# Kernel optimization log

Measured on AMD Instinct MI355X. Metric: run time of the kernel, lower is better.

The kernel has to match this reference:

```python
import jax, jax.numpy as jnp
import numpy as np

B, S, E = 4, 2048, 1024
N, H = 16, 64  # n_head, per-head hidden


def setup_inputs() -> dict:
    key = jax.random.key(0)
    k1, k2, k3, k4, k5 = jax.random.split(key, 5)
    scale_in = 1.0 / np.sqrt(E)
    scale_h = 1.0 / np.sqrt(N * H)
    return {
        "x": jax.random.normal(k1, (B, S, E), dtype=jnp.float32),
        "W_qkv": jax.random.uniform(k2, (E, 3 * N * H), minval=-scale_in, maxval=scale_in, dtype=jnp.float32),
        "b_qkv": jax.random.uniform(k3, (3 * N * H,), minval=-scale_in, maxval=scale_in, dtype=jnp.float32),
        "W_out": jax.random.uniform(k4, (N * H, E), minval=-scale_h, maxval=scale_h, dtype=jnp.float32),
        "b_out": jax.random.uniform(k5, (E,), minval=-scale_h, maxval=scale_h, dtype=jnp.float32),
    }


def reference(x, W_qkv, b_qkv, W_out, b_out):
    b, s, e = x.shape
    qkv = x @ W_qkv + b_qkv                      # [B,S,3NH]
    q, k, v = jnp.split(qkv, 3, axis=-1)
    q = q.reshape(b, s, N, H).transpose(0, 2, 1, 3)  # [B,N,S,H]
    k = k.reshape(b, s, N, H).transpose(0, 2, 1, 3)
    v = v.reshape(b, s, N, H).transpose(0, 2, 1, 3)
    inv_scale = jnp.asarray(1.0 / np.sqrt(H), dtype=x.dtype)
    attn = jnp.einsum('bnqh,bnkh->bnqk', q, k) * inv_scale  # [B,N,S,S]
    causal = jnp.tril(jnp.ones((s, s), dtype=bool))
    attn = jnp.where(causal[None, None], attn, jnp.asarray(-jnp.inf, dtype=attn.dtype))
    attn = jax.nn.softmax(attn, axis=-1)
    out = jnp.einsum('bnqk,bnkh->bnqh', attn, v)  # [B,N,S,H]
    out = out.transpose(0, 2, 1, 3).reshape(b, s, N * H)
    return out @ W_out + b_out
```

## Files before the change

### kernel.cpp

```cpp
#include <hip/hip_runtime.h>
#include <hip/hip_bf16.h>

typedef __attribute__((ext_vector_type(8))) short s16x8;
typedef __attribute__((ext_vector_type(4))) short s16x4;
typedef __attribute__((ext_vector_type(4))) float f32x4;

#define MFMA16(a, b, c) __builtin_amdgcn_mfma_f32_16x16x32_bf16(a, b, c, 0, 0, 0)

__device__ __forceinline__ short f2bf(float f) {
  unsigned int x = __builtin_bit_cast(unsigned int, f);
  x += 0x7fffu + ((x >> 16) & 1u);
  return (short)(x >> 16);
}

__device__ __forceinline__ int cperm(int k) {
  return ((k & 12) << 1) | ((k >> 4) << 2) | (k & 3);
}

#define LDT 40

__global__ void cvt_f32_bf16(const float* __restrict__ in, short* __restrict__ out, int n) {
  int idx = blockIdx.x * blockDim.x + threadIdx.x;
  int stride = gridDim.x * blockDim.x;
  for (int i = idx * 4; i < n; i += stride * 4) {
    float4 v = *(const float4*)(in + i);
    s16x4 o;
    o[0] = f2bf(v.x); o[1] = f2bf(v.y); o[2] = f2bf(v.z); o[3] = f2bf(v.w);
    *(s16x4*)(out + i) = o;
  }
}

__global__ __launch_bounds__(256) void gemm_qkv(
    const short* __restrict__ X, const short* __restrict__ W,
    const float* __restrict__ bias,
    short* __restrict__ Qo, short* __restrict__ Ko, short* __restrict__ Vo) {
  const int N = 3072, Kd = 1024;
  __shared__ short As[128 * LDT];
  __shared__ short Bs[128 * LDT];
  int t = threadIdx.x;
  int nTN = N / 128;
  int m0 = (blockIdx.x / nTN) * 128;
  int n0 = (blockIdx.x % nTN) * 128;
  int lane = t & 63, w = t >> 6;
  int wr = (w >> 1) * 64, wc = (w & 1) * 64;
  int r = lane & 15, g = lane >> 4;

  int ar = t >> 1;
  int ak = (t & 1) << 4;
  int bk = t & 31;
  int bc = (t >> 5) << 4;
  int cbk = cperm(bk);

  f32x4 acc[4][4];
  const f32x4 z4 = {0.f, 0.f, 0.f, 0.f};
#pragma unroll
  for (int i = 0; i < 4; ++i)
#pragma unroll
    for (int j = 0; j < 4; ++j) acc[i][j] = z4;

  for (int kt = 0; kt < Kd; kt += 32) {
    if (kt) __syncthreads();
    const short* xr = X + (size_t)(m0 + ar) * Kd + kt + ak;
    s16x8 va0 = *(const s16x8*)(xr);
    s16x8 va1 = *(const s16x8*)(xr + 8);
    short* Ad = &As[ar * LDT];
    *(s16x4*)(Ad + cperm(ak))      = __builtin_shufflevector(va0, va0, 0, 1, 2, 3);
    *(s16x4*)(Ad + cperm(ak + 4))  = __builtin_shufflevector(va0, va0, 4, 5, 6, 7);
    *(s16x4*)(Ad + cperm(ak + 8))  = __builtin_shufflevector(va1, va1, 0, 1, 2, 3);
    *(s16x4*)(Ad + cperm(ak + 12)) = __builtin_shufflevector(va1, va1, 4, 5, 6, 7);
    const short* wrp = W + (size_t)(kt + bk) * N + n0 + bc;
    s16x8 vb0 = *(const s16x8*)(wrp);
    s16x8 vb1 = *(const s16x8*)(wrp + 8);
#pragma unroll
    for (int i = 0; i < 8; ++i) Bs[(bc + i) * LDT + cbk] = vb0[i];
#pragma unroll
    for (int i = 0; i < 8; ++i) Bs[(bc + 8 + i) * LDT + cbk] = vb1[i];
    __syncthreads();

    s16x8 af[4], bfr[4];
#pragma unroll
    for (int mi = 0; mi < 4; ++mi)
      af[mi] = *(const s16x8*)(&As[(wr + mi * 16 + r) * LDT + g * 8]);
#pragma unroll
    for (int ni = 0; ni < 4; ++ni)
      bfr[ni] = *(const s16x8*)(&Bs[(wc + ni * 16 + r) * LDT + g * 8]);
#pragma unroll
    for (int mi = 0; mi < 4; ++mi)
#pragma unroll
      for (int ni = 0; ni < 4; ++ni)
        acc[mi][ni] = MFMA16(af[mi], bfr[ni], acc[mi][ni]);
  }

#pragma unroll
  for (int ni = 0; ni < 4; ++ni) {
    int col = n0 + wc + ni * 16 + r;
    float bv = bias[col];
    int which = col >> 10;
    int rem = col & 1023;
    int head = rem >> 6, h = rem & 63;
    short* dst = (which == 0) ? Qo : (which == 1) ? Ko : Vo;
    float qsc = (which == 0) ? 0.125f : 1.0f;
#pragma unroll
    for (int mi = 0; mi < 4; ++mi)
#pragma unroll
      for (int e = 0; e < 4; ++e) {
        int row = m0 + wr + mi * 16 + g * 4 + e;
        int b = row >> 11, s = row & 2047;
        dst[((size_t)(b * 16 + head) * 2048 + s) * 64 + h] = f2bf((acc[mi][ni][e] + bv) * qsc);
      }
  }
}

__global__ __launch_bounds__(256) void gemm_out(
    const short* __restrict__ X, const short* __restrict__ W,
    const float* __restrict__ bias, float* __restrict__ Out) {
  const int N = 1024, Kd = 1024;
  __shared__ short As[128 * LDT];
  __shared__ short Bs[128 * LDT];
  int t = threadIdx.x;
  int nTN = N / 128;
  int m0 = (blockIdx.x / nTN) * 128;
  int n0 = (blockIdx.x % nTN) * 128;
  int lane = t & 63, w = t >> 6;
  int wr = (w >> 1) * 64, wc = (w & 1) * 64;
  int r = lane & 15, g = lane >> 4;
  int ar = t >> 1, ak = (t & 1) << 4;
  int bk = t & 31, bc = (t >> 5) << 4;
  int cbk = cperm(bk);

  f32x4 acc[4][4];
  const f32x4 z4 = {0.f, 0.f, 0.f, 0.f};
#pragma unroll
  for (int i = 0; i < 4; ++i)
#pragma unroll
    for (int j = 0; j < 4; ++j) acc[i][j] = z4;

  for (int kt = 0; kt < Kd; kt += 32) {
    if (kt) __syncthreads();
    const short* xr = X + (size_t)(m0 + ar) * Kd + kt + ak;
    s16x8 va0 = *(const s16x8*)(xr);
    s16x8 va1 = *(const s16x8*)(xr + 8);
    short* Ad = &As[ar * LDT];
    *(s16x4*)(Ad + cperm(ak))      = __builtin_shufflevector(va0, va0, 0, 1, 2, 3);
    *(s16x4*)(Ad + cperm(ak + 4))  = __builtin_shufflevector(va0, va0, 4, 5, 6, 7);
    *(s16x4*)(Ad + cperm(ak + 8))  = __builtin_shufflevector(va1, va1, 0, 1, 2, 3);
    *(s16x4*)(Ad + cperm(ak + 12)) = __builtin_shufflevector(va1, va1, 4, 5, 6, 7);
    const short* wrp = W + (size_t)(kt + bk) * N + n0 + bc;
    s16x8 vb0 = *(const s16x8*)(wrp);
    s16x8 vb1 = *(const s16x8*)(wrp + 8);
#pragma unroll
    for (int i = 0; i < 8; ++i) Bs[(bc + i) * LDT + cbk] = vb0[i];
#pragma unroll
    for (int i = 0; i < 8; ++i) Bs[(bc + 8 + i) * LDT + cbk] = vb1[i];
    __syncthreads();

    s16x8 af[4], bfr[4];
#pragma unroll
    for (int mi = 0; mi < 4; ++mi)
      af[mi] = *(const s16x8*)(&As[(wr + mi * 16 + r) * LDT + g * 8]);
#pragma unroll
    for (int ni = 0; ni < 4; ++ni)
      bfr[ni] = *(const s16x8*)(&Bs[(wc + ni * 16 + r) * LDT + g * 8]);
#pragma unroll
    for (int mi = 0; mi < 4; ++mi)
#pragma unroll
      for (int ni = 0; ni < 4; ++ni)
        acc[mi][ni] = MFMA16(af[mi], bfr[ni], acc[mi][ni]);
  }

#pragma unroll
  for (int ni = 0; ni < 4; ++ni) {
    int col = n0 + wc + ni * 16 + r;
    float bv = bias[col];
#pragma unroll
    for (int mi = 0; mi < 4; ++mi)
#pragma unroll
      for (int e = 0; e < 4; ++e) {
        int row = m0 + wr + mi * 16 + g * 4 + e;
        Out[(size_t)row * N + col] = acc[mi][ni][e] + bv;
      }
  }
}

#define LDTV 72
__global__ __launch_bounds__(256) void attn(
    const short* __restrict__ Qb, const short* __restrict__ Kb,
    const short* __restrict__ Vb, short* __restrict__ Ob) {
  const int S = 2048, H = 64;
  int bid = blockIdx.x;
  int bn = bid & 63;
  int pr = bid >> 6;
  int batch = bn >> 4, head = bn & 15;
  int t = threadIdx.x, lane = t & 63, w = t >> 6;
  int r = lane & 15, g = lane >> 4;

  const short* Qh = Qb + (size_t)bn * S * H;
  const short* Kh = Kb + (size_t)bn * S * H;
  const short* Vh = Vb + (size_t)bn * S * H;

  __shared__ short Vs[64 * LDTV];

  int vr = lane;
  int hbase = w * 16;
  int vcol = ((vr >> 5) << 5) + cperm(vr & 31);
  const f32x4 z4 = {0.f, 0.f, 0.f, 0.f};

#pragma unroll
  for (int ph = 0; ph < 2; ++ph) {
    int qt = ph ? pr : (15 - pr);
    int q0 = qt * 128;
    int qw = q0 + w * 32;
    int ntiles = qt * 2 + 2;

    s16x8 qf[2][2];
#pragma unroll
    for (int n = 0; n < 2; ++n)
#pragma unroll
      for (int ks = 0; ks < 2; ++ks) {
        const short* qr = Qh + (size_t)(qw + n * 16 + r) * H + ks * 32 + g * 4;
        s16x4 lo = *(const s16x4*)(qr);
        s16x4 hi = *(const s16x4*)(qr + 16);
        qf[n][ks] = __builtin_shufflevector(lo, hi, 0, 1, 2, 3, 4, 5, 6, 7);
      }

    f32x4 o[2][4];
#pragma unroll
    for (int n = 0; n < 2; ++n)
#pragma unroll
      for (int hb = 0; hb < 4; ++hb) o[n][hb] = z4;
    float mrun[2] = {-__builtin_inff(), -__builtin_inff()};
    float lsum[2] = {0.f, 0.f};

    auto LOADK = [&](int kv0, s16x8 (&kf)[4][2]) {
#pragma unroll
      for (int mp = 0; mp < 4; ++mp)
#pragma unroll
        for (int ks = 0; ks < 2; ++ks) {
          const short* kr = Kh + (size_t)(kv0 + mp * 16 + r) * H + ks * 32 + g * 4;
          s16x4 lo = *(const s16x4*)(kr);
          s16x4 hi = *(const s16x4*)(kr + 16);
          kf[mp][ks] = __builtin_shufflevector(lo, hi, 0, 1, 2, 3, 4, 5, 6, 7);
        }
    };

    s16x8 v0 = *(const s16x8*)(Vh + (size_t)vr * H + hbase);
    s16x8 v1 = *(const s16x8*)(Vh + (size_t)vr * H + hbase + 8);
    s16x8 kfA[4][2], kfB[4][2];
    LOADK(0, kfA);

    auto TILE = [&](int tt, s16x8 (&kfc)[4][2], s16x8 (&kfn)[4][2]) {
      int kv0 = tt * 64;
      if (tt | ph) __syncthreads();
#pragma unroll
      for (int i = 0; i < 8; ++i) Vs[(hbase + i) * LDTV + vcol] = v0[i];
#pragma unroll
      for (int i = 0; i < 8; ++i) Vs[(hbase + 8 + i) * LDTV + vcol] = v1[i];
      __syncthreads();
      if (tt + 1 < ntiles) {
        const short* vp = Vh + (size_t)((tt + 1) * 64 + vr) * H + hbase;
        v0 = *(const s16x8*)(vp);
        v1 = *(const s16x8*)(vp + 8);
      }
      int tn = tt + 1;
      if (tn < ntiles && tn * 64 <= qw + 31) LOADK(tn * 64, kfn);
      if (kv0 > qw + 31) return;

      int mpmax = (qw + 31 - kv0) >> 4; if (mpmax > 3) mpmax = 3;
      bool need_mask = (kv0 + 63 > qw);

      float p[4][2][4];
      float rmax[2] = {-__builtin_inff(), -__builtin_inff()};
#pragma unroll
      for (int mp = 0; mp < 4; ++mp) {
        if (mp <= mpmax) {
          f32x4 st[2] = {z4, z4};
#pragma unroll
          for (int n = 0; n < 2; ++n)
#pragma unroll
            for (int ks = 0; ks < 2; ++ks)
              st[n] = MFMA16(kfc[mp][ks], qf[n][ks], st[n]);
#pragma unroll
          for (int n = 0; n < 2; ++n)
#pragma unroll
            for (int e = 0; e < 4; ++e) {
              float v = st[n][e];
              if (need_mask) {
                int kv = kv0 + mp * 16 + g * 4 + e;
                int q = qw + n * 16 + r;
                if (kv > q) v = -__builtin_inff();
              }
              p[mp][n][e] = v;
              rmax[n] = fmaxf(rmax[n], v);
            }
        } else {
#pragma unroll
          for (int n = 0; n < 2; ++n)
#pragma unroll
            for (int e = 0; e < 4; ++e) p[mp][n][e] = 0.f;
        }
      }

#pragma unroll
      for (int n = 0; n < 2; ++n) {
        rmax[n] = fmaxf(rmax[n], __shfl_xor(rmax[n], 16));
        rmax[n] = fmaxf(rmax[n], __shfl_xor(rmax[n], 32));
      }

#pragma unroll
      for (int n = 0; n < 2; ++n) {
        if (!__all(rmax[n] - mrun[n] <= 8.0f)) {
          float mnew = fmaxf(mrun[n], rmax[n]);
          float sc = __expf(mrun[n] - mnew);
          lsum[n] *= sc;
          mrun[n] = mnew;
#pragma unroll
          for (int e = 0; e < 4; ++e) {
            float bs = __shfl(sc, (lane & 48) + g * 4 + e);
#pragma unroll
            for (int hb = 0; hb < 4; ++hb) o[n][hb][e] *= bs;
          }
        }
      }

#pragma unroll
      for (int mp = 0; mp < 4; ++mp) {
        if (mp <= mpmax) {
#pragma unroll
          for (int n = 0; n < 2; ++n)
#pragma unroll
            for (int e = 0; e < 4; ++e) {
              float ev = __expf(p[mp][n][e] - mrun[n]);
              p[mp][n][e] = ev;
              lsum[n] += ev;
            }
        }
      }

      int kvhmax = mpmax >> 1;
#pragma unroll
      for (int kvh = 0; kvh < 2; ++kvh) {
        if (kvh > kvhmax) break;
        s16x8 pa[2];
#pragma unroll
        for (int n = 0; n < 2; ++n) {
          s16x8 tmp = {f2bf(p[2 * kvh][n][0]),     f2bf(p[2 * kvh][n][1]),
                       f2bf(p[2 * kvh][n][2]),     f2bf(p[2 * kvh][n][3]),
                       f2bf(p[2 * kvh + 1][n][0]), f2bf(p[2 * kvh + 1][n][1]),
                       f2bf(p[2 * kvh + 1][n][2]), f2bf(p[2 * kvh + 1][n][3])};
          pa[n] = tmp;
        }
#pragma unroll
        for (int hb = 0; hb < 4; ++hb) {
          s16x8 vf = *(const s16x8*)(&Vs[(hb * 16 + r) * LDTV + kvh * 32 + g * 8]);
#pragma unroll
          for (int n = 0; n < 2; ++n) o[n][hb] = MFMA16(pa[n], vf, o[n][hb]);
        }
      }
    };

    for (int tt = 0; tt < ntiles; tt += 2) {
      TILE(tt, kfA, kfB);
      TILE(tt + 1, kfB, kfA);
    }

#pragma unroll
    for (int n = 0; n < 2; ++n) {
      float lt = lsum[n];
      lt += __shfl_xor(lt, 16);
      lt += __shfl_xor(lt, 32);
      float il = 1.0f / lt;
#pragma unroll
      for (int e = 0; e < 4; ++e) {
        float bv = __shfl(il, (lane & 48) + g * 4 + e);
        int s = qw + n * 16 + g * 4 + e;
#pragma unroll
        for (int hb = 0; hb < 4; ++hb) {
          int c = head * 64 + hb * 16 + r;
          Ob[(size_t)(batch * 2048 + s) * 1024 + c] = f2bf(o[n][hb][e] * bv);
        }
      }
    }
  }
}

extern "C" void kernel_launch(void* const* d_in, const int* in_sizes, int n_in,
                              void* d_out, int out_size, void* d_ws, size_t ws_size,
                              hipStream_t stream) {
  const float* x    = (const float*)d_in[0];
  const float* Wqkv = (const float*)d_in[1];
  const float* bqkv = (const float*)d_in[2];
  const float* Wout = (const float*)d_in[3];
  const float* bout = (const float*)d_in[4];
  float* out = (float*)d_out;

  char* ws = (char*)d_ws;
  short* Xb    = (short*)(ws);
  short* Wqkvb = (short*)(ws + ((size_t)16 << 20));
  short* Woutb = (short*)(ws + ((size_t)22 << 20));
  short* Qb    = (short*)(ws + ((size_t)24 << 20));
  short* Kb    = (short*)(ws + ((size_t)40 << 20));
  short* Vb    = (short*)(ws + ((size_t)56 << 20));

  cvt_f32_bf16<<<2048, 256, 0, stream>>>(x, Xb, 4 * 2048 * 1024);
  cvt_f32_bf16<<<1024, 256, 0, stream>>>(Wqkv, Wqkvb, 1024 * 3072);
  cvt_f32_bf16<<<512, 256, 0, stream>>>(Wout, Woutb, 1024 * 1024);

  gemm_qkv<<<64 * 24, 256, 0, stream>>>(Xb, Wqkvb, bqkv, Qb, Kb, Vb);
  attn<<<512, 256, 0, stream>>>(Qb, Kb, Vb, Xb);
  gemm_out<<<64 * 8, 256, 0, stream>>>(Xb, Woutb, bout, out);
}
```

Before: 283.5 us.

## Pre-permute Q/K and write V transposed in QKV GEMM epilogue; drop LDS staging

The QKV projection epilogue now writes Q and K with a column permutation so attention can load MFMA fragments with a single 16-byte load, and writes V transposed and permuted so attention loads V fragments straight from global memory. The attention kernel drops its shared-memory V staging and the two barriers per tile. The softmax scale now includes log2(e) so exponentials use exp2f. The trade-off is strided scattered stores in the GEMM epilogue for V, and V loads that are no longer prefetched a tile ahead, which may expose global latency.

Measured after the change: 299.0 us. 1.05x slower.

```diff
diff --git a/kernel.cpp b/kernel.cpp
--- a/kernel.cpp
+++ b/kernel.cpp
@@ -99,14 +99,20 @@
     int rem = col & 1023;
     int head = rem >> 6, h = rem & 63;
     short* dst = (which == 0) ? Qo : (which == 1) ? Ko : Vo;
-    float qsc = (which == 0) ? 0.125f : 1.0f;
+    float qsc = (which == 0) ? 0.125f * 1.44269504f : 1.0f;
+    int hp = (h & 32) | cperm(h & 31);
 #pragma unroll
     for (int mi = 0; mi < 4; ++mi)
 #pragma unroll
       for (int e = 0; e < 4; ++e) {
         int row = m0 + wr + mi * 16 + g * 4 + e;
         int b = row >> 11, s = row & 2047;
-        dst[((size_t)(b * 16 + head) * 2048 + s) * 64 + h] = f2bf((acc[mi][ni][e] + bv) * qsc);
+        size_t idx;
+        if (which == 2)
+          idx = ((size_t)(b * 16 + head) * 64 + h) * 2048 + ((s & ~31) | cperm(s & 31));
+        else
+          idx = ((size_t)(b * 16 + head) * 2048 + s) * 64 + hp;
+        dst[idx] = f2bf((acc[mi][ni][e] + bv) * qsc);
       }
   }
 }
@@ -182,10 +188,9 @@
   }
 }
 
-#define LDTV 72
 __global__ __launch_bounds__(256) void attn(
     const short* __restrict__ Qb, const short* __restrict__ Kb,
-    const short* __restrict__ Vb, short* __restrict__ Ob) {
+    const short* __restrict__ Vt, short* __restrict__ Ob) {
   const int S = 2048, H = 64;
   int bid = blockIdx.x;
   int bn = bid & 63;
@@ -196,13 +201,7 @@
 
   const short* Qh = Qb + (size_t)bn * S * H;
   const short* Kh = Kb + (size_t)bn * S * H;
-  const short* Vh = Vb + (size_t)bn * S * H;
-
-  __shared__ short Vs[64 * LDTV];
-
-  int vr = lane;
-  int hbase = w * 16;
-  int vcol = ((vr >> 5) << 5) + cperm(vr & 31);
+  const short* Vh = Vt + (size_t)bn * S * H;
   const f32x4 z4 = {0.f, 0.f, 0.f, 0.f};
 
 #pragma unroll
@@ -216,12 +215,8 @@
 #pragma unroll
     for (int n = 0; n < 2; ++n)
 #pragma unroll
-      for (int ks = 0; ks < 2; ++ks) {
-        const short* qr = Qh + (size_t)(qw + n * 16 + r) * H + ks * 32 + g * 4;
-        s16x4 lo = *(const s16x4*)(qr);
-        s16x4 hi = *(const s16x4*)(qr + 16);
-        qf[n][ks] = __builtin_shufflevector(lo, hi, 0, 1, 2, 3, 4, 5, 6, 7);
-      }
+      for (int ks = 0; ks < 2; ++ks)
+        qf[n][ks] = *(const s16x8*)(Qh + (size_t)(qw + n * 16 + r) * H + ks * 32 + g * 8);
 
     f32x4 o[2][4];
 #pragma unroll
@@ -235,35 +230,26 @@
 #pragma unroll
       for (int mp = 0; mp < 4; ++mp)
 #pragma unroll
-        for (int ks = 0; ks < 2; ++ks) {
-          const short* kr = Kh + (size_t)(kv0 + mp * 16 + r) * H + ks * 32 + g * 4;
-          s16x4 lo = *(const s16x4*)(kr);
-          s16x4 hi = *(const s16x4*)(kr + 16);
-          kf[mp][ks] = __builtin_shufflevector(lo, hi, 0, 1, 2, 3, 4, 5, 6, 7);
-        }
+        for (int ks = 0; ks < 2; ++ks)
+          kf[mp][ks] = *(const s16x8*)(Kh + (size_t)(kv0 + mp * 16 + r) * H + ks * 32 + g * 8);
     };
 
-    s16x8 v0 = *(const s16x8*)(Vh + (size_t)vr * H + hbase);
-    s16x8 v1 = *(const s16x8*)(Vh + (size_t)vr * H + hbase + 8);
     s16x8 kfA[4][2], kfB[4][2];
     LOADK(0, kfA);
 
     auto TILE = [&](int tt, s16x8 (&kfc)[4][2], s16x8 (&kfn)[4][2]) {
       int kv0 = tt * 64;
-      if (tt | ph) __syncthreads();
-#pragma unroll
-      for (int i = 0; i < 8; ++i) Vs[(hbase + i) * LDTV + vcol] = v0[i];
-#pragma unroll
-      for (int i = 0; i < 8; ++i) Vs[(hbase + 8 + i) * LDTV + vcol] = v1[i];
-      __syncthreads();
-      if (tt + 1 < ntiles) {
-        const short* vp = Vh + (size_t)((tt + 1) * 64 + vr) * H + hbase;
-        v0 = *(const s16x8*)(vp);
-        v1 = *(const s16x8*)(vp + 8);
-      }
+      if (kv0 > qw + 31) return;
+
+      s16x8 vf[2][4];
+#pragma unroll
+      for (int kvh = 0; kvh < 2; ++kvh)
+#pragma unroll
+        for (int hb = 0; hb < 4; ++hb)
+          vf[kvh][hb] = *(const s16x8*)(Vh + (size_t)(hb * 16 + r) * S + kv0 + kvh * 32 + g * 8);
+
       int tn = tt + 1;
       if (tn < ntiles && tn * 64 <= qw + 31) LOADK(tn * 64, kfn);
-      if (kv0 > qw + 31) return;
 
       int mpmax = (qw + 31 - kv0) >> 4; if (mpmax > 3) mpmax = 3;
       bool need_mask = (kv0 + 63 > qw);
@@ -310,7 +296,7 @@
       for (int n = 0; n < 2; ++n) {
         if (!__all(rmax[n] - mrun[n] <= 8.0f)) {
           float mnew = fmaxf(mrun[n], rmax[n]);
-          float sc = __expf(mrun[n] - mnew);
+          float sc = exp2f(mrun[n] - mnew);
           lsum[n] *= sc;
           mrun[n] = mnew;
 #pragma unroll
@@ -329,7 +315,7 @@
           for (int n = 0; n < 2; ++n)
 #pragma unroll
             for (int e = 0; e < 4; ++e) {
-              float ev = __expf(p[mp][n][e] - mrun[n]);
+              float ev = exp2f(p[mp][n][e] - mrun[n]);
               p[mp][n][e] = ev;
               lsum[n] += ev;
             }
@@ -350,11 +336,9 @@
           pa[n] = tmp;
         }
 #pragma unroll
-        for (int hb = 0; hb < 4; ++hb) {
-          s16x8 vf = *(const s16x8*)(&Vs[(hb * 16 + r) * LDTV + kvh * 32 + g * 8]);
-#pragma unroll
-          for (int n = 0; n < 2; ++n) o[n][hb] = MFMA16(pa[n], vf, o[n][hb]);
-        }
+        for (int hb = 0; hb < 4; ++hb)
+#pragma unroll
+          for (int n = 0; n < 2; ++n) o[n][hb] = MFMA16(pa[n], vf[kvh][hb], o[n][hb]);
       }
     };
 
```
